# Kernel tuning notes

Measured on AMD Instinct MI355X. Metric: run time of the kernel, lower is better.

Reference implementation:

```python
import jax, jax.numpy as jnp
import numpy as np
import math

N = 4096      # nodes
E = 131072    # edges (avg degree 32)
C = 128       # input channels
RATIO = 0.5   # TopKPooling default ratio
DIMS = [(128, 256), (256, 512), (512, 512), (512, 256), (256, 128)]


def setup_inputs() -> dict:
    key = jax.random.key(0)
    ks = jax.random.split(key, 16)
    inp = {}
    inp['x'] = jax.random.normal(ks[0], (N, C), jnp.float32)
    inp['edge_index'] = jax.random.randint(ks[1], (2, E), 0, N, jnp.int32)
    for i, (fi, fo) in enumerate(DIMS):
        inp[f'w{i}'] = jax.random.normal(ks[2 + i], (fi, fo), jnp.float32) / np.sqrt(fi).astype(np.float32)
        inp[f'b{i}'] = jnp.zeros((fo,), jnp.float32)
    inp['p0'] = jax.random.normal(ks[10], (256,), jnp.float32)
    inp['p1'] = jax.random.normal(ks[11], (512,), jnp.float32)
    return inp


def _gcn(x, M, w, b):
    # GCNConv: add self loops (weight 1), symmetric D^-1/2 normalization with
    # deg computed over target (col) index, aggregate messages src->dst.
    # M[r, c] = weight of edge (src=r, dst=c); dense equivalent of sparse conv.
    n = M.shape[0]
    Mc = M + jnp.eye(n, dtype=M.dtype)
    deg = Mc.sum(axis=0)
    dis = jnp.where(deg > 0, jax.lax.rsqrt(deg), 0.0)
    A = dis[:, None] * Mc * dis[None, :]          # normalized (src, dst)
    return jax.nn.relu(A.T @ (x @ w) + b)          # out[dst] = sum_src A * xW


def _augment(M):
    # augment_adj: add self loops then spspmm(A, A) -> dense (M+I) @ (M+I)
    B = M + jnp.eye(M.shape[0], dtype=M.dtype)
    return B @ B


def _pool(x, M, p):
    # TopKPooling: score = tanh(x.p / ||p||), keep top ceil(ratio*n) nodes,
    # gate kept features by score, slice adjacency to kept nodes.
    s = jnp.tanh((x @ p) / jnp.linalg.norm(p))
    k = int(math.ceil(RATIO * x.shape[0]))
    vals, perm = jax.lax.top_k(s, k)
    return x[perm] * vals[:, None], M[perm][:, perm], perm


def reference(x, edge_index, w0, b0, w1, b1, w2, b2, w3, b3, w4, b4, p0, p1):
    # dense adjacency M[src, dst] from edge list with unit edge weights
    M = jnp.zeros((N, N), jnp.float32).at[edge_index[0], edge_index[1]].add(1.0)

    # down block 0
    x = _gcn(x, M, w0, b0)
    res0, M0 = x, M
    x, M, perm0 = _pool(x, _augment(M), p0)

    # down block 1
    x = _gcn(x, M, w1, b1)
    res1, M1 = x, M
    x, M, perm1 = _pool(x, _augment(M), p1)

    # bottleneck
    x = _gcn(x, M, w2, b2)

    # up block 1: scatter into zeros, sum residual
    up = jnp.zeros_like(res1).at[perm1].set(x)
    x = _gcn(res1 + up, M1, w3, b3)

    # up block 0
    up = jnp.zeros_like(res0).at[perm0].set(x)
    x = _gcn(res0 + up, M0, w4, b4)
    return x
```

## Files before the change

kernel.cpp:

```cpp
#include <hip/hip_runtime.h>

#define NN 4096
#define EE 131072
#define NP1 2048
#define NP2 1024

typedef __attribute__((ext_vector_type(8))) __bf16 bf16x8;
typedef __attribute__((ext_vector_type(4))) float f32x4;
typedef __attribute__((ext_vector_type(8))) unsigned short ushort8;

static __device__ inline unsigned short bfbits(__bf16 b) {
  union { __bf16 x; unsigned short u; } c; c.x = b; return c.u;
}
static __device__ inline void split2(float v, unsigned short& h, unsigned short& l) {
  __bf16 hb = (__bf16)v;
  float hf = (float)hb;
  __bf16 lb = (__bf16)(v - hf);
  h = bfbits(hb); l = bfbits(lb);
}

static __device__ inline size_t pchunk(int r, int k, int NT) {
  return ((size_t)(r >> 4) * NT + (k >> 5)) * 64 + (((k >> 3) & 3) << 4) + (r & 15);
}

static __device__ inline void tsplit_body(const float* in, unsigned short* oh, unsigned short* ol,
                                          int R, int C, int c) {
  int lane = c & 63, tile = c >> 6;
  int NT = R >> 5;
  int kt = tile % NT, jt = tile / NT;
  int j = jt * 16 + (lane & 15);
  int k = kt * 32 + (lane >> 4) * 8;
  ushort8 hv, lv;
#pragma unroll
  for (int e = 0; e < 8; ++e) {
    unsigned short he, le;
    split2(in[(size_t)(k + e) * C + j], he, le);
    hv[e] = he; lv[e] = le;
  }
  *(ushort8*)&oh[(size_t)c * 8] = hv;
  *(ushort8*)&ol[(size_t)c * 8] = lv;
}


__global__ __launch_bounds__(256) void prep_all(
    const int* __restrict__ esrc, const int* __restrict__ edst,
    int* __restrict__ cnt_src, int* __restrict__ cnt_dst,
    const float* w0, const float* w1, const float* w2, const float* w3, const float* w4,
    unsigned short* o0h, unsigned short* o0l, unsigned short* o1h, unsigned short* o1l,
    unsigned short* o2h, unsigned short* o2l, unsigned short* o3h, unsigned short* o3l,
    unsigned short* o4h, unsigned short* o4l,
    const float* p0, const float* p1, float* pnrm) {
  __shared__ float red[4];
  int b = blockIdx.x;
  int tid = threadIdx.x;
  if (b < EE / 256) {
    int e = b * 256 + tid;
    atomicAdd(&cnt_src[esrc[e]], 1);
    atomicAdd(&cnt_dst[edst[e]], 1);
  } else if (b < EE / 256 + 288) {
    int g = (b - EE / 256) * 256 + tid;
    if (g < 4096)        tsplit_body(w0, o0h, o0l, 128, 256, g);
    else if (g < 20480)  tsplit_body(w1, o1h, o1l, 256, 512, g - 4096);
    else if (g < 53248)  tsplit_body(w2, o2h, o2l, 512, 512, g - 20480);
    else if (g < 69632)  tsplit_body(w3, o3h, o3l, 512, 256, g - 53248);
    else                 tsplit_body(w4, o4h, o4l, 256, 128, g - 69632);
  } else {
    int which = b - (EE / 256 + 288);
    const float* p = which ? p1 : p0;
    int C = which ? 512 : 256;
    float acc = 0.f;
    for (int j = tid; j < C; j += 256) { float v = p[j]; acc += v * v; }
    for (int o = 32; o > 0; o >>= 1) acc += __shfl_down(acc, o);
    if ((tid & 63) == 0) red[tid >> 6] = acc;
    __syncthreads();
    if (tid == 0) pnrm[which] = sqrtf(red[0] + red[1] + red[2] + red[3]);
  }
}

__global__ __launch_bounds__(1024) void scan2(const int* __restrict__ cnt_dst,
                                              const int* __restrict__ cnt_src,
                                              int* __restrict__ csc_off, int* __restrict__ csr_off,
                                              float* __restrict__ dis0, int n) {
  __shared__ int tmp[4096];
  const int* in = blockIdx.x ? cnt_src : cnt_dst;
  int* out = blockIdx.x ? csr_off : csc_off;
  int tid = threadIdx.x;
  for (int i = tid; i < n; i += 1024) {
    int v = in[i];
    tmp[i] = v;
    if (blockIdx.x == 0) dis0[i] = rsqrtf((float)v + 1.0f);
  }
  __syncthreads();
  for (int off = 1; off < n; off <<= 1) {
    int v[4];
    int c = 0;
    for (int i = tid; i < n; i += 1024) { v[c++] = (i >= off) ? tmp[i - off] : 0; }
    __syncthreads();
    c = 0;
    for (int i = tid; i < n; i += 1024) { tmp[i] += v[c++]; }
    __syncthreads();
  }
  for (int i = tid; i < n; i += 1024) out[i + 1] = tmp[i];
  if (tid == 0) out[0] = 0;
}

__global__ void scatter_kernel(const int* __restrict__ src, const int* __restrict__ dst,
                               const int* __restrict__ csc_off, const int* __restrict__ csr_off,
                               int* __restrict__ fill_dst, int* __restrict__ fill_src,
                               int* __restrict__ csc_src, int* __restrict__ csr_dst, int E) {
  int e = blockIdx.x * blockDim.x + threadIdx.x;
  if (e < E) {
    int s = src[e], d = dst[e];
    int p = atomicAdd(&fill_dst[d], 1);
    csc_src[csc_off[d] + p] = s;
    int q = atomicAdd(&fill_src[s], 1);
    csr_dst[csr_off[s] + q] = d;
  }
}


__global__ void score_key(const float* __restrict__ X, const float* __restrict__ p,
                          const float* __restrict__ pn, float* __restrict__ s,
                          unsigned long long* __restrict__ keys, int C) {
  int i = blockIdx.x;
  int tid = threadIdx.x;
  float acc = 0.f;
  for (int j = tid; j < C; j += 256) acc += X[(size_t)i * C + j] * p[j];
  for (int o = 32; o > 0; o >>= 1) acc += __shfl_down(acc, o);
  __shared__ float red[4];
  if ((tid & 63) == 0) red[tid >> 6] = acc;
  __syncthreads();
  if (tid == 0) {
    float sv = tanhf((red[0] + red[1] + red[2] + red[3]) / pn[0]);
    s[i] = sv;
    unsigned u = __float_as_uint(sv);
    unsigned m = (u & 0x80000000u) ? ~u : (u | 0x80000000u);
    keys[i] = (((unsigned long long)(~m)) << 32) | (unsigned)i;
  }
}

__global__ __launch_bounds__(256) void rank_count(const unsigned long long* __restrict__ keys,
                                                  int* __restrict__ rank) {
  __shared__ unsigned long long kk[512];
  int tid = threadIdx.x;
  int cand = blockIdx.x * 256 + tid;
  int base = blockIdx.y * 512;
  kk[tid] = keys[base + tid];
  kk[tid + 256] = keys[base + tid + 256];
  __syncthreads();
  unsigned long long kc = keys[cand];
  int c = 0;
#pragma unroll 8
  for (int t = 0; t < 512; ++t) c += (kk[t] < kc) ? 1 : 0;
  atomicAdd(&rank[cand], c);
}

__global__ void rank_place(const float* __restrict__ s, const int* __restrict__ rank, int k, int n,
                           int* __restrict__ kept, int* __restrict__ perm, float* __restrict__ vals,
                           int* __restrict__ cntk) {
  int i = blockIdx.x * blockDim.x + threadIdx.x;
  if (i < n) {
    int r = rank[i];
    int isk = (r < k) ? 1 : 0;
    if (isk) { perm[r] = i; vals[r] = s[i]; kept[i] = r; }
    else kept[i] = -1;
    if (cntk) cntk[i] = isk;
  }
}

__global__ void pool_tsplit_p(const float* __restrict__ X, const int* __restrict__ perm,
                              const float* __restrict__ vals, const float* __restrict__ dis,
                              unsigned short* __restrict__ h, unsigned short* __restrict__ l) {
  int c = blockIdx.x * blockDim.x + threadIdx.x;
  int tile = c >> 6, lno = c & 63;
  int kt = tile & 63, jt = tile >> 6;
  int j = jt * 16 + (lno & 15);
  int k0 = kt * 32 + (lno >> 4) * 8;
  ushort8 hv, lv;
#pragma unroll
  for (int e = 0; e < 8; ++e) {
    int node = k0 + e;
    float sc = vals[node] * dis[node];
    float v = X[(size_t)perm[node] * 256 + j] * sc;
    unsigned short he, le;
    split2(v, he, le);
    hv[e] = he; lv[e] = le;
  }
  *(ushort8*)&h[(size_t)c * 8] = hv;
  *(ushort8*)&l[(size_t)c * 8] = lv;
}

__global__ __launch_bounds__(256) void pool1_misc(
    const float* __restrict__ res1, const int* __restrict__ perm1, const float* __restrict__ vals1,
    unsigned short* __restrict__ x2h, unsigned short* __restrict__ x2l,
    const unsigned short* __restrict__ B1rm, const unsigned short* __restrict__ B1t,
    unsigned short* __restrict__ Gh2, unsigned short* __restrict__ Hh2) {
  int b = blockIdx.x;
  int tid = threadIdx.x;
  if (b < 256) {
    int c = b * 256 + tid;
    int lane = c & 63, tile = c >> 6;
    int kt = tile & 15, rt = tile >> 4;
    int r = rt * 16 + (lane & 15);
    int k0 = kt * 32 + (lane >> 4) * 8;
    float v = vals1[r];
    const float* src = res1 + (size_t)perm1[r] * 512 + k0;
    ushort8 hv, lv;
#pragma unroll
    for (int e = 0; e < 8; ++e) {
      unsigned short he, le;
      split2(src[e] * v, he, le);
      hv[e] = he; lv[e] = le;
    }
    *(ushort8*)&x2h[(size_t)c * 8] = hv;
    *(ushort8*)&x2l[(size_t)c * 8] = lv;
  } else {
    int idx = b - 256;
    int mat = idx >> 10;
    int c = (idx & 1023) * 256 + tid;
    const unsigned short* in = mat ? B1t : B1rm;
    unsigned short* outp = mat ? Hh2 : Gh2;
    const int NT = NP1 >> 5;
    int lane = c & 63, tile = c >> 6;
    int kt = tile % NT, at = tile / NT;
    int a = at * 16 + (lane & 15);
    int sub = lane >> 4;
    int p = perm1[a];
    size_t sc = ((size_t)(p >> 4) * NT + kt) * 64 + sub * 16 + (p & 15);
    *(ushort8*)&outp[(size_t)c * 8] = *(const ushort8*)&in[sc * 8];
  }
}


__global__ __launch_bounds__(256) void augcnt(const int* __restrict__ csr_off,
                                              const int* __restrict__ csr_dst,
                                              const int* __restrict__ kept,
                                              const int* __restrict__ perm,
                                              unsigned short* __restrict__ rm,
                                              const int* __restrict__ esrc,
                                              const int* __restrict__ edst,
                                              int* __restrict__ cntk) {
  __shared__ float acc[NP1];
  int b = blockIdx.x;
  if (b < NP1) {
    int ki = b;
    int r = perm[ki];
    for (int t = threadIdx.x; t < NP1; t += 256) acc[t] = 0.f;
    __syncthreads();
    int s = csr_off[r], e = csr_off[r + 1];
    int nm = e - s;
    int wave = threadIdx.x >> 6, lane = threadIdx.x & 63;
    for (int m = wave; m <= nm; m += 4) {
      int k = (m < nm) ? csr_dst[s + m] : r;
      int s2 = csr_off[k], e2 = csr_off[k + 1];
      int n2 = e2 - s2;
      for (int t = lane; t <= n2; t += 64) {
        int j = (t < n2) ? csr_dst[s2 + t] : k;
        int kj = kept[j];
        if (kj >= 0) atomicAdd(&acc[kj], 1.0f);
      }
    }
    __syncthreads();
    if (threadIdx.x == 0) acc[ki] += 1.0f;
    __syncthreads();
    int tid = threadIdx.x;
    ushort8 hv;
#pragma unroll
    for (int e8 = 0; e8 < 8; ++e8) hv[e8] = bfbits((__bf16)acc[tid * 8 + e8]);
    size_t dst = (((size_t)(ki >> 4)) * 64 + (tid >> 2)) * 64 + (size_t)(tid & 3) * 16 + (ki & 15);
    *(ushort8*)&rm[dst * 8] = hv;
  } else {
    int e = (b - NP1) * 256 + threadIdx.x;
    if (kept[esrc[e]] >= 0) atomicAdd(&cntk[edst[e]], 1);
  }
}

__global__ __launch_bounds__(256) void degtp(const unsigned short* __restrict__ in,
                                             unsigned short* __restrict__ outp, int n,
                                             const int* __restrict__ csc_off,
                                             const int* __restrict__ csc_src,
                                             const int* __restrict__ cntk,
                                             const int* __restrict__ perm,
                                             float* __restrict__ dis) {
  __shared__ unsigned short t[64][72];
  int b = blockIdx.x;
  if (b < 1024) {
    int r0 = (b >> 5) * 64, c0 = (b & 31) * 64;
    int NT = n >> 5;
    for (int q = threadIdx.x; q < 512; q += 256) {
      int lt = q >> 6, l = q & 63;
      int rt = lt >> 1, kt2 = lt & 1;
      int r = rt * 16 + (l & 15), k = kt2 * 32 + (l >> 4) * 8;
      ushort8 v = *(const ushort8*)&in[pchunk(r0 + r, c0 + k, NT) * 8];
      *(ushort8*)&t[r][k] = v;
    }
    __syncthreads();
    for (int q = threadIdx.x; q < 512; q += 256) {
      int lt = q >> 6, l = q & 63;
      int jt = lt >> 1, kt2 = lt & 1;
      int j = jt * 16 + (l & 15), k = kt2 * 32 + (l >> 4) * 8;
      ushort8 v;
#pragma unroll
      for (int e = 0; e < 8; ++e) v[e] = t[k + e][j];
      *(ushort8*)&outp[pchunk(c0 + j, r0 + k, NT) * 8] = v;
    }
  } else {
    int bid = b - 1024;
    int wid = threadIdx.x >> 6, lane = threadIdx.x & 63;
    int c = bid * 4 + wid;
    int r = perm[c];
    int s = csc_off[r], e = csc_off[r + 1];
    int sum = 0;
    for (int t2 = s + lane; t2 < e; t2 += 64) sum += cntk[csc_src[t2]];
    for (int o = 32; o > 0; o >>= 1) sum += __shfl_down(sum, o);
    if (lane == 0) dis[c] = rsqrtf((float)(sum + cntk[r] + 1));
  }
}


template <int C>
__global__ __launch_bounds__(256) void spmm_presplit(const float* __restrict__ X,
                                                     const int* __restrict__ off,
                                                     const int* __restrict__ srcs,
                                                     const float* __restrict__ dis,
                                                     unsigned short* __restrict__ h,
                                                     unsigned short* __restrict__ l) {
  __shared__ float buf[4][C];
  constexpr int VEC = C / 64;
  int w = threadIdx.x >> 6, lane = threadIdx.x & 63;
  int c = blockIdx.x * 4 + w;
  int j = lane * VEC;
  float dc = dis[c];
  float acc[VEC];
  const float* p = X + (size_t)c * C + j;
#pragma unroll
  for (int u = 0; u < VEC; ++u) acc[u] = dc * p[u];
  int s = off[c], e = off[c + 1];
  for (int t = s; t < e; ++t) {
    int sr = srcs[t];
    float ds = dis[sr];
    const float* q = X + (size_t)sr * C + j;
#pragma unroll
    for (int u = 0; u < VEC; ++u) acc[u] += ds * q[u];
  }
#pragma unroll
  for (int u = 0; u < VEC; ++u) buf[w][j + u] = dc * acc[u];
  __syncthreads();
  constexpr int NC = C / 8;
  if (lane < NC) {
    const float* src = &buf[w][lane * 8];
    ushort8 hv, lv;
#pragma unroll
    for (int e2 = 0; e2 < 8; ++e2) {
      unsigned short he, le;
      split2(src[e2], he, le);
      hv[e2] = he; lv[e2] = le;
    }
    size_t ch = pchunk(c, lane * 8, C >> 5);
    *(ushort8*)&h[ch * 8] = hv;
    *(ushort8*)&l[ch * 8] = lv;
  }
}

template <int C>
__global__ __launch_bounds__(256) void spmm_gather_v(const float* __restrict__ Y,
                                                     const int* __restrict__ off,
                                                     const int* __restrict__ srcs,
                                                     const float* __restrict__ dis,
                                                     const float* __restrict__ bias,
                                                     float* __restrict__ out) {
  constexpr int VEC = C / 64;
  int w = threadIdx.x >> 6, lane = threadIdx.x & 63;
  int c = blockIdx.x * 4 + w;
  int j = lane * VEC;
  float acc[VEC];
  const float* p = Y + (size_t)c * C + j;
#pragma unroll
  for (int u = 0; u < VEC; ++u) acc[u] = p[u];
  int s = off[c], e = off[c + 1];
  for (int t = s; t < e; ++t) {
    const float* q = Y + (size_t)srcs[t] * C + j;
#pragma unroll
    for (int u = 0; u < VEC; ++u) acc[u] += q[u];
  }
  float d = dis[c];
  float* o = out + (size_t)c * C + j;
#pragma unroll
  for (int u = 0; u < VEC; ++u) o[u] = fmaxf(d * acc[u] + bias[j + u], 0.0f);
}


template <int S>
__global__ void ep_zsplit(const float* __restrict__ p, unsigned short* __restrict__ h,
                          unsigned short* __restrict__ l, int M, int N) {
  int t = blockIdx.x * blockDim.x + threadIdx.x;
  int tile = t >> 6, w = t & 63;
  int NT = N >> 5;
  int rt = tile / NT, kt = tile % NT;
  int r = rt * 16 + (w & 15);
  int k = kt * 32 + (w >> 4) * 8;
  const float* p0 = p + (size_t)r * N + k;
  ushort8 hv, lv;
#pragma unroll
  for (int e = 0; e < 8; ++e) {
    float v = p0[e];
#pragma unroll
    for (int s = 1; s < S; ++s) v += p0[(size_t)s * M * N + e];
    unsigned short he, le;
    split2(v, he, le);
    hv[e] = he; lv[e] = le;
  }
  *(ushort8*)&h[(size_t)t * 8] = hv;
  *(ushort8*)&l[(size_t)t * 8] = lv;
}

template <int S, int RSQ>
__global__ void unpool_ep_split(const float* __restrict__ res, const float* __restrict__ pscr,
                                const int* __restrict__ kept, const float* __restrict__ rs,
                                const float* __restrict__ bias,
                                unsigned short* __restrict__ h, unsigned short* __restrict__ l,
                                int M, int C) {
  int c = blockIdx.x * blockDim.x + threadIdx.x;
  int lane = c & 63, tile = c >> 6;
  int NT = C >> 5;
  int kt = tile % NT, rt = tile / NT;
  int r = rt * 16 + (lane & 15);
  int j0 = kt * 32 + (lane >> 4) * 8;
  int kv = kept[r];
  float rsv = 0.f;
  if (kv >= 0) { rsv = rs[kv]; if (RSQ) rsv = rsqrtf(rsv); }
  ushort8 hv, lv;
#pragma unroll
  for (int e = 0; e < 8; ++e) {
    float v = res[(size_t)r * C + j0 + e];
    if (kv >= 0) {
      float a = 0.f;
#pragma unroll
      for (int s = 0; s < S; ++s) a += pscr[((size_t)s * M + kv) * C + j0 + e];
      v += fmaxf(rsv * a + bias[j0 + e], 0.0f);
    }
    unsigned short he, le;
    split2(v, he, le);
    hv[e] = he; lv[e] = le;
  }
  *(ushort8*)&h[(size_t)c * 8] = hv;
  *(ushort8*)&l[(size_t)c * 8] = lv;
}

template <int S>
__global__ void ep_aug_cs2(const float* __restrict__ p, unsigned short* __restrict__ th,
                           unsigned short* __restrict__ tl, float* __restrict__ deg, int n) {
  int c = blockIdx.x * 256 + threadIdx.x;
  int r0 = blockIdx.y * 64;
  int NT = n >> 5;
  float cs = 0.f;
  for (int g = 0; g < 8; ++g) {
    float vbuf[8];
#pragma unroll
    for (int e = 0; e < 8; ++e) {
      int r = r0 + g * 8 + e;
      float v = 0.f;
#pragma unroll
      for (int s = 0; s < S; ++s) v += p[((size_t)s * n + r) * n + c];
      if (r == c) v += 1.0f;
      vbuf[e] = v;
      cs += v;
    }
    ushort8 hv, lv;
#pragma unroll
    for (int e = 0; e < 8; ++e) {
      unsigned short he, le;
      split2(vbuf[e], he, le);
      hv[e] = he; lv[e] = le;
    }
    size_t ch = pchunk(c, r0 + g * 8, NT);
    *(ushort8*)&th[ch * 8] = hv;
    *(ushort8*)&tl[ch * 8] = lv;
  }
  atomicAdd(&deg[c], cs);
}

template <int EPI, int AL, int BL, int KK, int S, int RSQ>
__global__ __launch_bounds__(256) void gemm16(
    const unsigned short* __restrict__ Ah, const unsigned short* __restrict__ Al,
    const unsigned short* __restrict__ Bh, const unsigned short* __restrict__ Bl,
    int M, int N, const float* __restrict__ rs, const float* __restrict__ bias,
    float* __restrict__ C, unsigned short* __restrict__ Th, unsigned short* __restrict__ Tl) {
  static_assert(KK % 32 == 0, "K");
  constexpr int KSTEPS = KK / 32;
  const int NT = (KK * S) >> 5;
  const int gx = gridDim.x;
  int id = blockIdx.y * gx + blockIdx.x;
  int cpx = (gx * gridDim.y) >> 3;
  int sid = (id & 7) * cpx + (id >> 3);
  const int bx = sid % gx, by = sid / gx;
  const int z = (S > 1) ? blockIdx.z : 0;
  const int wid = threadIdx.x >> 6, lane = threadIdx.x & 63;
  const int i0 = by * 64 + (wid >> 1) * 32;
  const int j0 = bx * 64 + (wid & 1) * 32;
  const int lr = lane & 15, lk = lane >> 4;
  size_t aoff[2], boff[2];
#pragma unroll
  for (int t = 0; t < 2; ++t) {
    aoff[t] = ((size_t)((i0 >> 4) + t) * NT + z * (KK >> 5)) * 512 + lane * 8;
    boff[t] = ((size_t)((j0 >> 4) + t) * NT + z * (KK >> 5)) * 512 + lane * 8;
  }
  const f32x4 zf = {0.f, 0.f, 0.f, 0.f};
  f32x4 acc[2][2];
  acc[0][0] = zf; acc[0][1] = zf; acc[1][0] = zf; acc[1][1] = zf;

  bf16x8 ahf[4][2], bhf[4][2], alf[4][2], blf[4][2];
  auto loadk = [&](int kk, int b) {
    size_t o = (size_t)kk * 512;
    ahf[b][0] = *(const bf16x8*)(Ah + aoff[0] + o);
    ahf[b][1] = *(const bf16x8*)(Ah + aoff[1] + o);
    bhf[b][0] = *(const bf16x8*)(Bh + boff[0] + o);
    bhf[b][1] = *(const bf16x8*)(Bh + boff[1] + o);
    if constexpr (AL) {
      alf[b][0] = *(const bf16x8*)(Al + aoff[0] + o);
      alf[b][1] = *(const bf16x8*)(Al + aoff[1] + o);
    }
    if constexpr (BL) {
      blf[b][0] = *(const bf16x8*)(Bl + boff[0] + o);
      blf[b][1] = *(const bf16x8*)(Bl + boff[1] + o);
    }
  };
  auto domm = [&](int b) {
#pragma unroll
    for (int am = 0; am < 2; ++am)
#pragma unroll
      for (int bn = 0; bn < 2; ++bn) {
        acc[am][bn] = __builtin_amdgcn_mfma_f32_16x16x32_bf16(ahf[b][am], bhf[b][bn], acc[am][bn], 0, 0, 0);
        if constexpr (BL)
          acc[am][bn] = __builtin_amdgcn_mfma_f32_16x16x32_bf16(ahf[b][am], blf[b][bn], acc[am][bn], 0, 0, 0);
        if constexpr (AL)
          acc[am][bn] = __builtin_amdgcn_mfma_f32_16x16x32_bf16(alf[b][am], bhf[b][bn], acc[am][bn], 0, 0, 0);
      }
  };

  loadk(0, 0);
  if constexpr (KSTEPS > 1) loadk(1, 1);
  if constexpr (KSTEPS > 2) loadk(2, 2);
#pragma unroll
  for (int kk = 0; kk < KSTEPS; ++kk) {
    const int cur = kk & 3;
    if (kk + 3 < KSTEPS) loadk(kk + 3, (cur + 3) & 3);
    domm(cur);
  }

#pragma unroll
  for (int am = 0; am < 2; ++am)
#pragma unroll
    for (int bn = 0; bn < 2; ++bn) {
      int ib = i0 + 16 * am + lk * 4;
      int j = j0 + 16 * bn + lr;
      f32x4 a = acc[am][bn];
      if constexpr (S > 1) {
#pragma unroll
        for (int r = 0; r < 4; ++r) C[((size_t)z * M + ib + r) * N + j] = a[r];
      } else if constexpr (EPI == 0) {
#pragma unroll
        for (int r = 0; r < 4; ++r) C[(size_t)(ib + r) * N + j] = a[r];
      } else if constexpr (EPI == 1) {
#pragma unroll
        for (int r = 0; r < 4; ++r) {
          float rsv = rs[ib + r];
          if (RSQ) rsv = rsqrtf(rsv);
          C[(size_t)(ib + r) * N + j] = rsv * a[r];
        }
      } else if constexpr (EPI == 2) {
        unsigned long long hp = 0, lp = 0;
#pragma unroll
        for (int r = 0; r < 4; ++r) {
          float rsv = rs[ib + r];
          if (RSQ) rsv = rsqrtf(rsv);
          unsigned short hv, lv;
          split2(rsv * a[r], hv, lv);
          hp |= ((unsigned long long)hv) << (16 * r);
          lp |= ((unsigned long long)lv) << (16 * r);
        }
        size_t c = pchunk(j, ib, M >> 5);
        *(unsigned long long*)&Th[c * 8 + (ib & 7)] = hp;
        *(unsigned long long*)&Tl[c * 8 + (ib & 7)] = lp;
      } else if constexpr (EPI == 3) {
#pragma unroll
        for (int r = 0; r < 4; ++r) {
          float rsv = rs[ib + r];
          if (RSQ) rsv = rsqrtf(rsv);
          C[(size_t)(ib + r) * N + j] = fmaxf(rsv * a[r] + bias[j], 0.0f);
        }
      } else {
#pragma unroll
        for (int r = 0; r < 4; ++r)
          C[(size_t)(ib + r) * N + j] = fmaxf(a[r] + bias[j], 0.0f);
      }
    }
}

template <int AL, int BL, int KK, int S>
__global__ __launch_bounds__(256) void gemm64(
    const unsigned short* __restrict__ Ah, const unsigned short* __restrict__ Al,
    const unsigned short* __restrict__ Bh, const unsigned short* __restrict__ Bl,
    int M, int N, float* __restrict__ C) {
  static_assert(KK % 32 == 0, "K");
  constexpr int KSTEPS = KK / 32;
  const int NT = (KK * S) >> 5;
  const int gx = gridDim.x;
  int id = blockIdx.y * gx + blockIdx.x;
  int cpx = (gx * gridDim.y) >> 3;
  int sid = (id & 7) * cpx + (id >> 3);
  const int bx = sid % gx, by = sid / gx;
  const int z = blockIdx.z;
  const int wid = threadIdx.x >> 6, lane = threadIdx.x & 63;
  const int i0 = by * 128 + (wid >> 1) * 64;
  const int j0 = bx * 128 + (wid & 1) * 64;
  const int lr = lane & 15, lk = lane >> 4;
  size_t aoff[4], boff[4];
#pragma unroll
  for (int t = 0; t < 4; ++t) {
    aoff[t] = ((size_t)((i0 >> 4) + t) * NT + z * (KK >> 5)) * 512 + lane * 8;
    boff[t] = ((size_t)((j0 >> 4) + t) * NT + z * (KK >> 5)) * 512 + lane * 8;
  }
  const f32x4 zf = {0.f, 0.f, 0.f, 0.f};
  f32x4 acc[4][4];
#pragma unroll
  for (int a = 0; a < 4; ++a)
#pragma unroll
    for (int b = 0; b < 4; ++b) acc[a][b] = zf;

  bf16x8 ahf[2][4], bhf[2][4], alf[2][4], blf[2][4];
  auto loadk = [&](int kk, int b) {
    size_t o = (size_t)kk * 512;
#pragma unroll
    for (int t = 0; t < 4; ++t) {
      ahf[b][t] = *(const bf16x8*)(Ah + aoff[t] + o);
      bhf[b][t] = *(const bf16x8*)(Bh + boff[t] + o);
      if constexpr (AL) alf[b][t] = *(const bf16x8*)(Al + aoff[t] + o);
      if constexpr (BL) blf[b][t] = *(const bf16x8*)(Bl + boff[t] + o);
    }
  };
  auto domm = [&](int b) {
#pragma unroll
    for (int am = 0; am < 4; ++am)
#pragma unroll
      for (int bn = 0; bn < 4; ++bn) {
        acc[am][bn] = __builtin_amdgcn_mfma_f32_16x16x32_bf16(ahf[b][am], bhf[b][bn], acc[am][bn], 0, 0, 0);
        if constexpr (BL)
          acc[am][bn] = __builtin_amdgcn_mfma_f32_16x16x32_bf16(ahf[b][am], blf[b][bn], acc[am][bn], 0, 0, 0);
        if constexpr (AL)
          acc[am][bn] = __builtin_amdgcn_mfma_f32_16x16x32_bf16(alf[b][am], bhf[b][bn], acc[am][bn], 0, 0, 0);
      }
  };

  loadk(0, 0);
#pragma unroll
  for (int kk = 0; kk < KSTEPS; ++kk) {
    const int cur = kk & 1;
    if (kk + 1 < KSTEPS) loadk(kk + 1, cur ^ 1);
    domm(cur);
  }

#pragma unroll
  for (int am = 0; am < 4; ++am)
#pragma unroll
    for (int bn = 0; bn < 4; ++bn) {
      int ib = i0 + 16 * am + lk * 4;
      int j = j0 + 16 * bn + lr;
      f32x4 a = acc[am][bn];
#pragma unroll
      for (int r = 0; r < 4; ++r) C[((size_t)z * M + ib + r) * N + j] = a[r];
    }
}


extern "C" void kernel_launch(void* const* d_in, const int* in_sizes, int n_in,
                              void* d_out, int out_size, void* d_ws, size_t ws_size,
                              hipStream_t stream) {
  (void)in_sizes; (void)n_in; (void)out_size; (void)ws_size;
  const float* x  = (const float*)d_in[0];
  const int* ei   = (const int*)d_in[1];
  const int* esrc = ei;
  const int* edst = ei + EE;
  const float* w0 = (const float*)d_in[2];
  const float* b0 = (const float*)d_in[3];
  const float* w1 = (const float*)d_in[4];
  const float* b1 = (const float*)d_in[5];
  const float* w2 = (const float*)d_in[6];
  const float* b2 = (const float*)d_in[7];
  const float* w3 = (const float*)d_in[8];
  const float* b3 = (const float*)d_in[9];
  const float* w4 = (const float*)d_in[10];
  const float* b4 = (const float*)d_in[11];
  const float* p0 = (const float*)d_in[12];
  const float* p1 = (const float*)d_in[13];
  float* out = (float*)d_out;

  char* ws = (char*)d_ws;
  size_t off = 0;
  auto alloc = [&](size_t b) { void* p = ws + off; off += (b + 255) & ~(size_t)255; return p; };

  int* csc_off = (int*)alloc(4 * (NN + 1));
  int* csr_off = (int*)alloc(4 * (NN + 1));
  int* csc_src = (int*)alloc(4 * EE);
  int* csr_dst = (int*)alloc(4 * EE);

  size_t zero_bytes = 4 * NN * 4 + 4 * NP2 + 4 * NN + 4 * NP1;
  int* cnts    = (int*)alloc(zero_bytes);
  int* cnt_dst = cnts;
  int* cnt_src = cnts + NN;
  int* fill_dst = cnts + 2 * NN;
  int* fill_src = cnts + 3 * NN;
  float* deg2 = (float*)(cnts + 4 * NN);
  int* rank0 = (int*)(deg2 + NP2);
  int* rank1 = rank0 + NN;

  int* cntk  = (int*)alloc(4 * NN);
  int* kept0 = (int*)alloc(4 * NN);
  int* perm0 = (int*)alloc(4 * NP1);
  int* kept1 = (int*)alloc(4 * NP1);
  int* perm1 = (int*)alloc(4 * NP2);
  float* dis0 = (float*)alloc(4 * NN);
  float* dis1 = (float*)alloc(4 * NP1);
  float* pnrm = (float*)alloc(8);
  float* s0   = (float*)alloc(4 * NN);
  float* vals0 = (float*)alloc(4 * NP1);
  float* s1   = (float*)alloc(4 * NP1);
  float* vals1 = (float*)alloc(4 * NP2);
  unsigned long long* keys0 = (unsigned long long*)alloc(8 * NN);
  unsigned long long* keys1 = (unsigned long long*)alloc(8 * NP1);

  const size_t MB = 1024 * 1024;
  char* regB1 = (char*)alloc(16 * MB);
  unsigned short* Gh2 = (unsigned short*)regB1;
  unsigned short* Hh2 = (unsigned short*)(regB1 + 4 * MB);
  unsigned short* B2th = (unsigned short*)(regB1 + 4 * MB);
  unsigned short* B2tl = (unsigned short*)(regB1 + 6 * MB);
  float* pscr = (float*)alloc(16 * MB);

  unsigned short* B1rm = (unsigned short*)alloc(8 * MB);
  unsigned short* B1t  = (unsigned short*)alloc(8 * MB);
  float* res0 = (float*)alloc(4 * MB);
  float* res1 = (float*)alloc(4 * MB);
  float* yreg = (float*)alloc(4 * MB);
  char* ytreg = (char*)alloc(4 * MB);
  unsigned short* Y2th = (unsigned short*)ytreg;
  unsigned short* Y2tl = (unsigned short*)(ytreg + 1 * MB);
  unsigned short* Y3th = (unsigned short*)ytreg;
  unsigned short* Y3tl = (unsigned short*)(ytreg + 1 * MB);
  char* xsreg = (char*)alloc(4 * MB);
  unsigned short* x3h = (unsigned short*)xsreg;
  unsigned short* x3l = (unsigned short*)(xsreg + 2 * MB);
  unsigned short* x4h = (unsigned short*)xsreg;
  unsigned short* x4l = (unsigned short*)(xsreg + 2 * MB);
  unsigned short* xh = (unsigned short*)alloc(1 * MB);
  unsigned short* xl = (unsigned short*)alloc(1 * MB);
  char* xsm = (char*)alloc(2 * MB);
  unsigned short* x1th = (unsigned short*)xsm;
  unsigned short* x1tl = (unsigned short*)(xsm + 1 * MB);
  unsigned short* Zh = (unsigned short*)xsm;
  unsigned short* Zl = (unsigned short*)(xsm + 1 * MB);
  unsigned short* x2h = (unsigned short*)xsm;
  unsigned short* x2l = (unsigned short*)(xsm + 1 * MB);
  unsigned short* Wt0h = (unsigned short*)alloc(256 * 128 * 2);
  unsigned short* Wt0l = (unsigned short*)alloc(256 * 128 * 2);
  unsigned short* Wt1h = (unsigned short*)alloc(512 * 256 * 2);
  unsigned short* Wt1l = (unsigned short*)alloc(512 * 256 * 2);
  unsigned short* Wt2h = (unsigned short*)alloc(512 * 512 * 2);
  unsigned short* Wt2l = (unsigned short*)alloc(512 * 512 * 2);
  unsigned short* Wt3h = (unsigned short*)alloc(256 * 512 * 2);
  unsigned short* Wt3l = (unsigned short*)alloc(256 * 512 * 2);
  unsigned short* Wt4h = (unsigned short*)alloc(128 * 256 * 2);
  unsigned short* Wt4l = (unsigned short*)alloc(128 * 256 * 2);

  hipMemsetAsync(cnts, 0, zero_bytes, stream);

  prep_all<<<EE / 256 + 288 + 2, 256, 0, stream>>>(
      esrc, edst, cnt_src, cnt_dst, w0, w1, w2, w3, w4,
      Wt0h, Wt0l, Wt1h, Wt1l, Wt2h, Wt2l, Wt3h, Wt3l, Wt4h, Wt4l, p0, p1, pnrm);
  scan2<<<2, 1024, 0, stream>>>(cnt_dst, cnt_src, csc_off, csr_off, dis0, NN);
  scatter_kernel<<<EE / 256, 256, 0, stream>>>(esrc, edst, csc_off, csr_off,
                                               fill_dst, fill_src, csc_src, csr_dst, EE);

  spmm_presplit<128><<<NN / 4, 256, 0, stream>>>(x, csc_off, csc_src, dis0, xh, xl);
  gemm16<4, 1, 1, 128, 1, 0><<<dim3(4, 64), 256, 0, stream>>>(xh, xl, Wt0h, Wt0l,
                                                              NN, 256, nullptr, b0, res0, nullptr, nullptr);

  score_key<<<NN, 256, 0, stream>>>(res0, p0, pnrm + 0, s0, keys0, 256);
  rank_count<<<dim3(NN / 256, NN / 512), 256, 0, stream>>>(keys0, rank0);
  rank_place<<<NN / 256, 256, 0, stream>>>(s0, rank0, NP1, NN, kept0, perm0, vals0, cntk);

  augcnt<<<NP1 + EE / 256, 256, 0, stream>>>(csr_off, csr_dst, kept0, perm0, B1rm,
                                             esrc, edst, cntk);
  degtp<<<1024 + NP1 / 4, 256, 0, stream>>>(B1rm, B1t, NP1, csc_off, csc_src, cntk, perm0, dis1);

  pool_tsplit_p<<<(NP1 * 256 / 8) / 256, 256, 0, stream>>>(res0, perm0, vals0, dis1, x1th, x1tl);
  gemm16<0, 0, 1, 1024, 2, 0><<<dim3(4, 32, 2), 256, 0, stream>>>(B1t, nullptr, x1th, x1tl,
                                                                  NP1, 256, nullptr, nullptr, pscr, nullptr, nullptr);
  ep_zsplit<2><<<(NP1 * 256 / 8) / 256, 256, 0, stream>>>(pscr, Zh, Zl, NP1, 256);
  gemm16<3, 1, 1, 256, 1, 0><<<dim3(8, 32), 256, 0, stream>>>(Zh, Zl, Wt1h, Wt1l,
                                                              NP1, 512, dis1, b1, res1, nullptr, nullptr);

  score_key<<<NP1, 256, 0, stream>>>(res1, p1, pnrm + 1, s1, keys1, 512);
  rank_count<<<dim3(NP1 / 256, NP1 / 512), 256, 0, stream>>>(keys1, rank1);
  rank_place<<<NP1 / 256, 256, 0, stream>>>(s1, rank1, NP2, NP1, kept1, perm1, vals1, nullptr);

  pool1_misc<<<256 + 2048, 256, 0, stream>>>(res1, perm1, vals1, x2h, x2l,
                                             B1rm, B1t, Gh2, Hh2);

  gemm64<0, 0, 512, 4><<<dim3(8, 8, 4), 256, 0, stream>>>(Gh2, nullptr, Hh2, nullptr,
                                                          NP2, NP2, pscr);
  ep_aug_cs2<4><<<dim3(NP2 / 256, NP2 / 64), 256, 0, stream>>>(pscr, B2th, B2tl, deg2, NP2);

  gemm16<2, 1, 1, 512, 1, 1><<<dim3(8, 16), 256, 0, stream>>>(x2h, x2l, Wt2h, Wt2l,
                                                              NP2, 512, deg2, nullptr, nullptr, Y2th, Y2tl);
  gemm16<0, 1, 1, 512, 2, 0><<<dim3(8, 16, 2), 256, 0, stream>>>(B2th, B2tl, Y2th, Y2tl,
                                                                 NP2, 512, nullptr, nullptr, pscr, nullptr, nullptr);

  unpool_ep_split<2, 1><<<(NP1 * 512 / 8) / 256, 256, 0, stream>>>(res1, pscr, kept1, deg2, b2,
                                                                   x3h, x3l, NP2, 512);
  gemm16<2, 1, 1, 512, 1, 0><<<dim3(4, 32), 256, 0, stream>>>(x3h, x3l, Wt3h, Wt3l,
                                                              NP1, 256, dis1, nullptr, nullptr, Y3th, Y3tl);
  gemm64<0, 1, 256, 8><<<dim3(2, 16, 8), 256, 0, stream>>>(B1t, nullptr, Y3th, Y3tl,
                                                           NP1, 256, pscr);

  unpool_ep_split<8, 0><<<(NN * 256 / 8) / 256, 256, 0, stream>>>(res0, pscr, kept0, dis1, b3,
                                                                  x4h, x4l, NP1, 256);
  gemm16<1, 1, 1, 256, 1, 0><<<dim3(2, 64), 256, 0, stream>>>(x4h, x4l, Wt4h, Wt4l,
                                                              NN, 128, dis0, nullptr, yreg, nullptr, nullptr);
  spmm_gather_v<128><<<NN / 4, 256, 0, stream>>>(yreg, csc_off, csc_src, dis0, b4, out);
}
```

Measured before the change: 312.5 us.

## Rework scan, widen rank_count grid, switch pooled aggregation to gemm64 split-K

The offset scan now gives each thread a 4-element chunk, does a 1024-wide shared-memory scan over the per-thread sums and writes local prefixes. This replaces a 4096-element log-step scan with many barriers. rank_count now compares against 256 keys per block instead of 512, which doubles the grid for more parallelism at the cost of more atomics. The first pooled adjacency multiply moves from gemm16 with 2-way split-K to gemm64 with 8-way split-K and bf16 hi/lo on the feature operand. That adds more partial-sum traffic in the epilogue reduction.

```diff
diff --git a/kernel.cpp b/kernel.cpp
--- a/kernel.cpp
+++ b/kernel.cpp
@@ -81,26 +81,30 @@
                                               const int* __restrict__ cnt_src,
                                               int* __restrict__ csc_off, int* __restrict__ csr_off,
                                               float* __restrict__ dis0, int n) {
-  __shared__ int tmp[4096];
+  __shared__ int part[1024];
   const int* in = blockIdx.x ? cnt_src : cnt_dst;
   int* out = blockIdx.x ? csr_off : csc_off;
   int tid = threadIdx.x;
-  for (int i = tid; i < n; i += 1024) {
-    int v = in[i];
-    tmp[i] = v;
-    if (blockIdx.x == 0) dis0[i] = rsqrtf((float)v + 1.0f);
-  }
+  int base = tid * 4;
+  int v[4];
+  int s = 0;
+#pragma unroll
+  for (int e = 0; e < 4; ++e) {
+    int x = in[base + e];
+    v[e] = x; s += x;
+    if (blockIdx.x == 0) dis0[base + e] = rsqrtf((float)x + 1.0f);
+  }
+  part[tid] = s;
   __syncthreads();
-  for (int off = 1; off < n; off <<= 1) {
-    int v[4];
-    int c = 0;
-    for (int i = tid; i < n; i += 1024) { v[c++] = (i >= off) ? tmp[i - off] : 0; }
+  for (int off2 = 1; off2 < 1024; off2 <<= 1) {
+    int t = (tid >= off2) ? part[tid - off2] : 0;
     __syncthreads();
-    c = 0;
-    for (int i = tid; i < n; i += 1024) { tmp[i] += v[c++]; }
+    part[tid] += t;
     __syncthreads();
   }
-  for (int i = tid; i < n; i += 1024) out[i + 1] = tmp[i];
+  int run = part[tid] - s;
+#pragma unroll
+  for (int e = 0; e < 4; ++e) { run += v[e]; out[base + e + 1] = run; }
   if (tid == 0) out[0] = 0;
 }
 
@@ -141,17 +145,16 @@
 
 __global__ __launch_bounds__(256) void rank_count(const unsigned long long* __restrict__ keys,
                                                   int* __restrict__ rank) {
-  __shared__ unsigned long long kk[512];
+  __shared__ unsigned long long kk[256];
   int tid = threadIdx.x;
   int cand = blockIdx.x * 256 + tid;
-  int base = blockIdx.y * 512;
+  int base = blockIdx.y * 256;
   kk[tid] = keys[base + tid];
-  kk[tid + 256] = keys[base + tid + 256];
   __syncthreads();
   unsigned long long kc = keys[cand];
   int c = 0;
 #pragma unroll 8
-  for (int t = 0; t < 512; ++t) c += (kk[t] < kc) ? 1 : 0;
+  for (int t = 0; t < 256; ++t) c += (kk[t] < kc) ? 1 : 0;
   atomicAdd(&rank[cand], c);
 }
 
@@ -786,7 +789,7 @@
                                                               NN, 256, nullptr, b0, res0, nullptr, nullptr);
 
   score_key<<<NN, 256, 0, stream>>>(res0, p0, pnrm + 0, s0, keys0, 256);
-  rank_count<<<dim3(NN / 256, NN / 512), 256, 0, stream>>>(keys0, rank0);
+  rank_count<<<dim3(NN / 256, NN / 256), 256, 0, stream>>>(keys0, rank0);
   rank_place<<<NN / 256, 256, 0, stream>>>(s0, rank0, NP1, NN, kept0, perm0, vals0, cntk);
 
   augcnt<<<NP1 + EE / 256, 256, 0, stream>>>(csr_off, csr_dst, kept0, perm0, B1rm,
@@ -794,14 +797,14 @@
   degtp<<<1024 + NP1 / 4, 256, 0, stream>>>(B1rm, B1t, NP1, csc_off, csc_src, cntk, perm0, dis1);
 
   pool_tsplit_p<<<(NP1 * 256 / 8) / 256, 256, 0, stream>>>(res0, perm0, vals0, dis1, x1th, x1tl);
-  gemm16<0, 0, 1, 1024, 2, 0><<<dim3(4, 32, 2), 256, 0, stream>>>(B1t, nullptr, x1th, x1tl,
-                                                                  NP1, 256, nullptr, nullptr, pscr, nullptr, nullptr);
-  ep_zsplit<2><<<(NP1 * 256 / 8) / 256, 256, 0, stream>>>(pscr, Zh, Zl, NP1, 256);
+  gemm64<0, 1, 256, 8><<<dim3(2, 16, 8), 256, 0, stream>>>(B1t, nullptr, x1th, x1tl,
+                                                           NP1, 256, pscr);
+  ep_zsplit<8><<<(NP1 * 256 / 8) / 256, 256, 0, stream>>>(pscr, Zh, Zl, NP1, 256);
   gemm16<3, 1, 1, 256, 1, 0><<<dim3(8, 32), 256, 0, stream>>>(Zh, Zl, Wt1h, Wt1l,
                                                               NP1, 512, dis1, b1, res1, nullptr, nullptr);
 
   score_key<<<NP1, 256, 0, stream>>>(res1, p1, pnrm + 1, s1, keys1, 512);
-  rank_count<<<dim3(NP1 / 256, NP1 / 512), 256, 0, stream>>>(keys1, rank1);
+  rank_count<<<dim3(NP1 / 256, NP1 / 256), 256, 0, stream>>>(keys1, rank1);
   rank_place<<<NP1 / 256, 256, 0, stream>>>(s1, rank1, NP2, NP1, kept1, perm1, vals1, nullptr);
 
   pool1_misc<<<256 + 2048, 256, 0, stream>>>(res1, perm1, vals1, x2h, x2l,
```

New measurement: 294.7 us. 5.7% less time.
